# Performance work log

Hardware: AMD Instinct MI355X
Metric: run time of the kernel (lower is better)

The kernel has to match this reference:

```python
import jax, jax.numpy as jnp
import numpy as np
import math

DIM_T = 1024   # time-embedding dim == hidden_size (required for the code to run)
HID = 1024
IN = 1024
LAYERS = 4
N = 4096


def sinusoidal_pos_emb(t, dim):
    half = dim // 2
    freqs = jnp.exp(jnp.arange(half, dtype=jnp.float32) * (-math.log(10000.0) / (half - 1)))
    ang = t.astype(jnp.float32)[:, None] * freqs[None, :]  # (N, half)
    return jnp.concatenate([jnp.sin(ang), jnp.cos(ang)], axis=-1)  # (N, dim)


def setup_inputs() -> dict:
    key = jax.random.key(0)
    ks = jax.random.split(key, 16)
    s = 0.02
    inp = {
        "x": jax.random.normal(ks[0], (N, IN), jnp.float32),
        "timesteps": jax.random.randint(ks[1], (N,), 0, 1000, jnp.int32),
        "proj_w": jax.random.normal(ks[2], (DIM_T, IN), jnp.float32) * s,
        "proj_b": jnp.zeros((DIM_T,), jnp.float32),
        "te_w1": jax.random.normal(ks[3], (DIM_T, DIM_T), jnp.float32) * s,
        "te_b1": jnp.zeros((DIM_T,), jnp.float32),
        "te_w2": jax.random.normal(ks[4], (DIM_T, DIM_T), jnp.float32) * s,
        "te_b2": jnp.zeros((DIM_T,), jnp.float32),
        # all layers take dim_t-sized input (layer i>0 still consumes x[i] per the source)
        "Wih": jax.random.normal(ks[5], (LAYERS, 4 * HID, DIM_T), jnp.float32) * s,
        "Whh": jax.random.normal(ks[6], (LAYERS, 4 * HID, HID), jnp.float32) * s,
        "bih": jnp.zeros((LAYERS, 4 * HID), jnp.float32),
        "bhh": jnp.zeros((LAYERS, 4 * HID), jnp.float32),
        "lin_w": jax.random.normal(ks[7], (IN, HID), jnp.float32) * s,
        "lin_b": jnp.zeros((IN,), jnp.float32),
    }
    return inp


def _lstm_cell(xi, h, c, Wih, Whh, bih, bhh):
    g = Wih @ xi + bih + Whh @ h + bhh  # (4H,)
    i, f, gg, o = jnp.split(g, 4)
    c2 = jax.nn.sigmoid(f) * c + jax.nn.sigmoid(i) * jnp.tanh(gg)
    h2 = jax.nn.sigmoid(o) * jnp.tanh(c2)
    return h2, c2


def reference(x, timesteps, proj_w, proj_b, te_w1, te_b1, te_w2, te_b2,
              Wih, Whh, bih, bhh, lin_w, lin_b):
    emb = sinusoidal_pos_emb(timesteps, DIM_T)
    emb = jax.nn.silu(emb @ te_w1.T + te_b1) @ te_w2.T + te_b2  # (N, dim_t)
    xp = x @ proj_w.T + proj_b + emb  # (N, dim_t)

    def sample_step(carry, xi):
        def layer_step(hc, lp):
            h, c = hc
            W1, W2, b1, b2 = lp
            return _lstm_cell(xi, h, c, W1, W2, b1, b2), None
        carry, _ = jax.lax.scan(layer_step, carry, (Wih, Whh, bih, bhh))
        h, _ = carry
        return carry, lin_w @ h + lin_b

    h0 = jnp.zeros((HID,), jnp.float32)
    c0 = jnp.zeros((HID,), jnp.float32)
    _, outputs = jax.lax.scan(sample_step, (h0, c0), xp)  # (N, IN)
    return outputs
```

## Files before the change

### kernel.cpp

```cpp
#include <hip/hip_runtime.h>
#include <hip/hip_bf16.h>
#include <stdint.h>

#define NS 4096
#define DT 1024
#define H4 4096

__device__ __forceinline__ float sigm_f(float x) { return 1.f / (1.f + __expf(-x)); }
__device__ __forceinline__ float tanh_f(float x) {
    float ax = fminf(fabsf(x), 15.f);
    float t = 1.f - 2.f / (__expf(2.f * ax) + 1.f);
    return copysignf(t, x);
}

__global__ void emb_kernel(const int* __restrict__ ts, float* __restrict__ emb) {
    int t = blockIdx.x;
    int i = threadIdx.x;
    float tv = (float)ts[t];
    const float c = -0.018024149455922082f;
    float f = __expf(c * (float)i);
    float a = tv * f;
    float s, co;
    sincosf(a, &s, &co);
    emb[(size_t)t * DT + i] = s;
    emb[(size_t)t * DT + 512 + i] = co;
}

template <bool SILU, bool SKIP, int XGMODE>
__global__ __launch_bounds__(256) void gemm_bt(
    const float* __restrict__ A, const float* __restrict__ B,
    const float* __restrict__ bias, const float* __restrict__ bias2,
    const float* __restrict__ skip, float* __restrict__ Cf,
    __hip_bfloat16* __restrict__ Cb, int M, int Nc, int K)
{
    __shared__ __align__(16) float As[16][132];
    __shared__ __align__(16) float Bs[16][68];
    const int bn = blockIdx.x, bm = blockIdx.y, lz = blockIdx.z;
    if (XGMODE) {
        B     += (size_t)lz * H4 * DT;
        bias  += (size_t)lz * H4;
        bias2 += (size_t)lz * H4;
    }
    const int tid = threadIdx.x;
    const int tr = tid >> 4, tc = tid & 15;
    const int alr = tid >> 1, alc = (tid & 1) << 3;
    const int blr = tid >> 2, blc = (tid & 3) << 2;
    const float* Ap = A + (size_t)(bm * 128 + alr) * K + alc;
    const float* Bp = B + (size_t)(bn * 64 + blr) * K + blc;

    float acc[8][4];
#pragma unroll
    for (int i = 0; i < 8; i++)
#pragma unroll
        for (int j = 0; j < 4; j++) acc[i][j] = 0.f;

    for (int kk = 0; kk < K; kk += 16) {
        float4 a0 = *(const float4*)(Ap + kk);
        float4 a1 = *(const float4*)(Ap + kk + 4);
        float4 b0 = *(const float4*)(Bp + kk);
        __syncthreads();
        As[alc + 0][alr] = a0.x; As[alc + 1][alr] = a0.y;
        As[alc + 2][alr] = a0.z; As[alc + 3][alr] = a0.w;
        As[alc + 4][alr] = a1.x; As[alc + 5][alr] = a1.y;
        As[alc + 6][alr] = a1.z; As[alc + 7][alr] = a1.w;
        Bs[blc + 0][blr] = b0.x; Bs[blc + 1][blr] = b0.y;
        Bs[blc + 2][blr] = b0.z; Bs[blc + 3][blr] = b0.w;
        __syncthreads();
#pragma unroll
        for (int k = 0; k < 16; k++) {
            const float4 av0 = *(const float4*)&As[k][tr * 8];
            const float4 av1 = *(const float4*)&As[k][tr * 8 + 4];
            const float4 bv  = *(const float4*)&Bs[k][tc * 4];
            float aa[8] = {av0.x, av0.y, av0.z, av0.w, av1.x, av1.y, av1.z, av1.w};
            float bb[4] = {bv.x, bv.y, bv.z, bv.w};
#pragma unroll
            for (int i = 0; i < 8; i++)
#pragma unroll
                for (int j = 0; j < 4; j++)
                    acc[i][j] = fmaf(aa[i], bb[j], acc[i][j]);
        }
    }

#pragma unroll
    for (int i = 0; i < 8; i++) {
        int row = bm * 128 + tr * 8 + i;
#pragma unroll
        for (int j = 0; j < 4; j++) {
            int col = bn * 64 + tc * 4 + j;
            float v = acc[i][j] + bias[col];
            if (XGMODE) v += bias2[col];
            if (SKIP)   v += skip[(size_t)row * Nc + col];
            if (SILU)   v = v * (1.f / (1.f + __expf(-v)));
            if (XGMODE) {
                int q = col >> 10, jj = col & 1023;
                size_t idx = (size_t)row * 16384 + (size_t)lz * 4096
                           + ((size_t)(jj >> 2) << 4) + (q << 2) + (jj & 3);
                if (XGMODE == 2) Cf[idx] = v;
                else             Cb[idx] = __float2bfloat16(v);
            } else {
                Cf[(size_t)row * Nc + col] = v;
            }
        }
    }
}

template <typename XT>
__global__ __launch_bounds__(256, 1) void seq_kernel(
    const float* __restrict__ Whh,
    const XT* __restrict__ XG,
    float* __restrict__ hall,
    uint64_t* hbuf)
{
    const int k = blockIdx.x;
    const int t = threadIdx.x;
    const int d = t >> 4, s = t & 15;
    const int q = d >> 2, r = d & 3;
    const int grow = q * 1024 + 4 * k + r;

    float w[4][64];
#pragma unroll
    for (int l = 0; l < 4; l++) {
        const float* src = Whh + ((size_t)l * H4 + grow) * 1024 + (s << 6);
#pragma unroll
        for (int c4 = 0; c4 < 16; c4++) {
            int ch = (c4 + s) & 15;
            float4 v = *(const float4*)(src + (ch << 2));
            w[l][c4 * 4 + 0] = v.x; w[l][c4 * 4 + 1] = v.y;
            w[l][c4 * 4 + 2] = v.z; w[l][c4 * 4 + 3] = v.w;
        }
    }

    __shared__ __align__(16) float lds_h[1024];
    __shared__ float lds_g[16];
    float creg = 0.f;

    for (int step = 0; step < NS; ++step) {
#pragma unroll
        for (int l = 0; l < 4; l++) {
            const int it = step * 4 + l + 1;
            const uint32_t rtag = (uint32_t)(it - 1);
            uint64_t* rb = (l & 1) ? (hbuf + 1024) : hbuf;
            uint64_t* wb = ((l + 1) & 1) ? (hbuf + 1024) : hbuf;

            uint32_t got = 0;
            int spins = 0;
            while (got != 0xFu) {
#pragma unroll
                for (int m = 0; m < 4; m++) {
                    if (!(got & (1u << m))) {
                        uint64_t u = __hip_atomic_load(&rb[(m << 8) + t],
                                                       __ATOMIC_RELAXED, __HIP_MEMORY_SCOPE_AGENT);
                        if ((uint32_t)u == rtag) {
                            lds_h[(m << 8) + t] = __uint_as_float((uint32_t)(u >> 32));
                            got |= (1u << m);
                        }
                    }
                }
                if (got != 0xFu && ++spins > 8) __builtin_amdgcn_s_sleep(1);
            }
            __syncthreads();

            float acc = 0.f;
            const float* hbase = &lds_h[s << 6];
#pragma unroll
            for (int c4 = 0; c4 < 16; c4++) {
                int ch = (c4 + s) & 15;
                const float4 hv = *(const float4*)(hbase + (ch << 2));
                acc = fmaf(w[l][c4 * 4 + 0], hv.x, acc);
                acc = fmaf(w[l][c4 * 4 + 1], hv.y, acc);
                acc = fmaf(w[l][c4 * 4 + 2], hv.z, acc);
                acc = fmaf(w[l][c4 * 4 + 3], hv.w, acc);
            }
            acc += __shfl_xor(acc, 1);
            acc += __shfl_xor(acc, 2);
            acc += __shfl_xor(acc, 4);
            acc += __shfl_xor(acc, 8);
            if (s == 0) {
                float xg = (float)XG[(size_t)(step * 4 + l) * H4 + (k << 4) + d];
                lds_g[d] = acc + xg;
            }
            __syncthreads();

            if (t < 4) {
                float gi = lds_g[t], gf = lds_g[4 + t], gg = lds_g[8 + t], go = lds_g[12 + t];
                float cn = sigm_f(gf) * creg + sigm_f(gi) * tanh_f(gg);
                creg = cn;
                float hn = sigm_f(go) * tanh_f(cn);
                if (l == 3) hall[(size_t)step * 1024 + (k << 2) + t] = hn;
                uint64_t word = ((uint64_t)__float_as_uint(hn) << 32) | (uint64_t)(uint32_t)it;
                __hip_atomic_store(&wb[(k << 2) + t], word,
                                   __ATOMIC_RELAXED, __HIP_MEMORY_SCOPE_AGENT);
            }
        }
    }
}

extern "C" void kernel_launch(void* const* d_in, const int* in_sizes, int n_in,
                              void* d_out, int out_size, void* d_ws, size_t ws_size,
                              hipStream_t stream)
{
    const float* x      = (const float*)d_in[0];
    const int*   ts     = (const int*)d_in[1];
    const float* proj_w = (const float*)d_in[2];
    const float* proj_b = (const float*)d_in[3];
    const float* te_w1  = (const float*)d_in[4];
    const float* te_b1  = (const float*)d_in[5];
    const float* te_w2  = (const float*)d_in[6];
    const float* te_b2  = (const float*)d_in[7];
    const float* Wih    = (const float*)d_in[8];
    const float* Whh    = (const float*)d_in[9];
    const float* bih    = (const float*)d_in[10];
    const float* bhh    = (const float*)d_in[11];
    const float* lin_w  = (const float*)d_in[12];
    const float* lin_b  = (const float*)d_in[13];
    float* out = (float*)d_out;

    char* ws = (char*)d_ws;
    const size_t MB16 = (size_t)NS * DT * 4;
    float* bufA = (float*)ws;
    float* bufB = (float*)(ws + MB16);
    const size_t xg_f32_bytes  = (size_t)NS * 16384 * 4;
    const size_t xg_bf16_bytes = (size_t)NS * 16384 * 2;
    const bool use_f32_xg = ws_size >= 2 * MB16 + xg_f32_bytes + 16384 + 64;
    float*          XGf = (float*)(ws + 2 * MB16);
    __hip_bfloat16* XGb = (__hip_bfloat16*)(ws + 2 * MB16);
    uint64_t* hbuf = (uint64_t*)(ws + 2 * MB16 +
                                 (use_f32_xg ? xg_f32_bytes : xg_bf16_bytes));

    hipMemsetAsync(hbuf, 0, 2 * 1024 * sizeof(uint64_t), stream);

    emb_kernel<<<NS, 512, 0, stream>>>(ts, bufA);
    gemm_bt<true, false, 0><<<dim3(16, 32), 256, 0, stream>>>(
        bufA, te_w1, te_b1, nullptr, nullptr, bufB, nullptr, NS, DT, DT);
    gemm_bt<false, false, 0><<<dim3(16, 32), 256, 0, stream>>>(
        bufB, te_w2, te_b2, nullptr, nullptr, bufA, nullptr, NS, DT, DT);
    gemm_bt<false, true, 0><<<dim3(16, 32), 256, 0, stream>>>(
        x, proj_w, proj_b, nullptr, bufA, bufB, nullptr, NS, DT, DT);
    if (use_f32_xg) {
        gemm_bt<false, false, 2><<<dim3(64, 32, 4), 256, 0, stream>>>(
            bufB, Wih, bih, bhh, nullptr, XGf, nullptr, NS, H4, DT);
        seq_kernel<float><<<256, 256, 0, stream>>>(Whh, XGf, bufA, hbuf);
    } else {
        gemm_bt<false, false, 1><<<dim3(64, 32, 4), 256, 0, stream>>>(
            bufB, Wih, bih, bhh, nullptr, nullptr, XGb, NS, H4, DT);
        seq_kernel<__hip_bfloat16><<<256, 256, 0, stream>>>(Whh, XGb, bufA, hbuf);
    }
    gemm_bt<false, false, 0><<<dim3(16, 32), 256, 0, stream>>>(
        bufA, lin_w, lin_b, nullptr, nullptr, out, nullptr, NS, DT, DT);
}
```

Before: 51.80 ms.

## Remap gate rows per wavefront to drop second barrier and prefetch XG

```diff
diff --git a/kernel.cpp b/kernel.cpp
--- a/kernel.cpp
+++ b/kernel.cpp
@@ -94,7 +94,7 @@
             if (XGMODE) {
                 int q = col >> 10, jj = col & 1023;
                 size_t idx = (size_t)row * 16384 + (size_t)lz * 4096
-                           + ((size_t)(jj >> 2) << 4) + (q << 2) + (jj & 3);
+                           + ((size_t)(jj >> 2) << 4) + ((jj & 3) << 2) + q;
                 if (XGMODE == 2) Cf[idx] = v;
                 else             Cb[idx] = __float2bfloat16(v);
             } else {
@@ -114,10 +114,12 @@
     const int k = blockIdx.x;
     const int t = threadIdx.x;
     const int d = t >> 4, s = t & 15;
-    const int q = d >> 2, r = d & 3;
+    const int q = d & 3, r = d >> 2;
+    const int ln = t & 63;
     const int grow = q * 1024 + 4 * k + r;
-
-    float w[4][64];
+    const int hrow = (k << 2) + r;
+
+    float wreg[4][64];
 #pragma unroll
     for (int l = 0; l < 4; l++) {
         const float* src = Whh + ((size_t)l * H4 + grow) * 1024 + (s << 6);
@@ -125,13 +127,12 @@
         for (int c4 = 0; c4 < 16; c4++) {
             int ch = (c4 + s) & 15;
             float4 v = *(const float4*)(src + (ch << 2));
-            w[l][c4 * 4 + 0] = v.x; w[l][c4 * 4 + 1] = v.y;
-            w[l][c4 * 4 + 2] = v.z; w[l][c4 * 4 + 3] = v.w;
-        }
-    }
-
-    __shared__ __align__(16) float lds_h[1024];
-    __shared__ float lds_g[16];
+            wreg[l][c4 * 4 + 0] = v.x; wreg[l][c4 * 4 + 1] = v.y;
+            wreg[l][c4 * 4 + 2] = v.z; wreg[l][c4 * 4 + 3] = v.w;
+        }
+    }
+
+    __shared__ __align__(16) float lds_h[2][1024];
     float creg = 0.f;
 
     for (int step = 0; step < NS; ++step) {
@@ -141,6 +142,22 @@
             const uint32_t rtag = (uint32_t)(it - 1);
             uint64_t* rb = (l & 1) ? (hbuf + 1024) : hbuf;
             uint64_t* wb = ((l + 1) & 1) ? (hbuf + 1024) : hbuf;
+            float* lh = lds_h[l & 1];
+
+            float xg0, xg1, xg2, xg3;
+            {
+                const XT* p = XG + (size_t)(it - 1) * H4 + (k << 4) + (r << 2);
+                if constexpr (sizeof(XT) == 4) {
+                    float4 v = *(const float4*)p;
+                    xg0 = v.x; xg1 = v.y; xg2 = v.z; xg3 = v.w;
+                } else {
+                    ushort4 v = *(const ushort4*)p;
+                    xg0 = __uint_as_float((uint32_t)v.x << 16);
+                    xg1 = __uint_as_float((uint32_t)v.y << 16);
+                    xg2 = __uint_as_float((uint32_t)v.z << 16);
+                    xg3 = __uint_as_float((uint32_t)v.w << 16);
+                }
+            }
 
             uint32_t got = 0;
             int spins = 0;
@@ -151,44 +168,47 @@
                         uint64_t u = __hip_atomic_load(&rb[(m << 8) + t],
                                                        __ATOMIC_RELAXED, __HIP_MEMORY_SCOPE_AGENT);
                         if ((uint32_t)u == rtag) {
-                            lds_h[(m << 8) + t] = __uint_as_float((uint32_t)(u >> 32));
+                            lh[(m << 8) + t] = __uint_as_float((uint32_t)(u >> 32));
                             got |= (1u << m);
                         }
                     }
                 }
-                if (got != 0xFu && ++spins > 8) __builtin_amdgcn_s_sleep(1);
+                if (got != 0xFu && ++spins > 16) __builtin_amdgcn_s_sleep(1);
             }
             __syncthreads();
 
             float acc = 0.f;
-            const float* hbase = &lds_h[s << 6];
+            const float* hbase = lh + (s << 6);
 #pragma unroll
             for (int c4 = 0; c4 < 16; c4++) {
                 int ch = (c4 + s) & 15;
                 const float4 hv = *(const float4*)(hbase + (ch << 2));
-                acc = fmaf(w[l][c4 * 4 + 0], hv.x, acc);
-                acc = fmaf(w[l][c4 * 4 + 1], hv.y, acc);
-                acc = fmaf(w[l][c4 * 4 + 2], hv.z, acc);
-                acc = fmaf(w[l][c4 * 4 + 3], hv.w, acc);
+                acc = fmaf(wreg[l][c4 * 4 + 0], hv.x, acc);
+                acc = fmaf(wreg[l][c4 * 4 + 1], hv.y, acc);
+                acc = fmaf(wreg[l][c4 * 4 + 2], hv.z, acc);
+                acc = fmaf(wreg[l][c4 * 4 + 3], hv.w, acc);
             }
             acc += __shfl_xor(acc, 1);
             acc += __shfl_xor(acc, 2);
             acc += __shfl_xor(acc, 4);
             acc += __shfl_xor(acc, 8);
-            if (s == 0) {
-                float xg = (float)XG[(size_t)(step * 4 + l) * H4 + (k << 4) + d];
-                lds_g[d] = acc + xg;
-            }
-            __syncthreads();
-
-            if (t < 4) {
-                float gi = lds_g[t], gf = lds_g[4 + t], gg = lds_g[8 + t], go = lds_g[12 + t];
-                float cn = sigm_f(gf) * creg + sigm_f(gi) * tanh_f(gg);
-                creg = cn;
-                float hn = sigm_f(go) * tanh_f(cn);
-                if (l == 3) hall[(size_t)step * 1024 + (k << 2) + t] = hn;
+
+            int q4 = ln >> 4;
+            float xa = (q4 & 2) ? ((q4 & 1) ? xg3 : xg2) : ((q4 & 1) ? xg1 : xg0);
+            float gval = acc + xa;
+
+            float gi = __shfl(gval, 0);
+            float gf = __shfl(gval, 16);
+            float gG = __shfl(gval, 32);
+            float go = __shfl(gval, 48);
+            float cn = sigm_f(gf) * creg + sigm_f(gi) * tanh_f(gG);
+            creg = cn;
+            float hn = sigm_f(go) * tanh_f(cn);
+
+            if (ln == 0) {
+                if (l == 3) hall[(size_t)step * 1024 + hrow] = hn;
                 uint64_t word = ((uint64_t)__float_as_uint(hn) << 32) | (uint64_t)(uint32_t)it;
-                __hip_atomic_store(&wb[(k << 2) + t], word,
+                __hip_atomic_store(&wb[hrow], word,
                                    __ATOMIC_RELAXED, __HIP_MEMORY_SCOPE_AGENT);
             }
         }
```

New measurement: 62.46 ms. 20.6% more time.
